# Kernel tuning notes

Measured on AMD Instinct MI355X. Metric: run time of the kernel, lower is better.

Reference implementation:

```python
import jax, jax.numpy as jnp
import numpy as np

EPS_DIST = 1e-8
EPS_BN = 1e-5


def _bn_relu(x, g, b):
    # training-mode BatchNorm1d over (batch, spatial) per channel, then ReLU
    mean = jnp.mean(x, axis=(0, 2), keepdims=True)
    var = jnp.mean((x - mean) ** 2, axis=(0, 2), keepdims=True)
    xhat = (x - mean) * jax.lax.rsqrt(var + EPS_BN)
    return jax.nn.relu(xhat * g[None, :, None] + b[None, :, None])


def setup_inputs() -> dict:
    key = jax.random.key(0)
    ks = jax.random.split(key, 8)
    B, N, M, C1, C2 = 8, 16384, 4096, 64, 256
    return {
        "p1": jax.random.normal(ks[0], (B, N, 3), jnp.float32),
        "p2": jax.random.normal(ks[1], (B, M, 3), jnp.float32),
        "f1": jax.random.normal(ks[2], (B, C1, N), jnp.float32),
        "f2": jax.random.normal(ks[3], (B, C2, M), jnp.float32),
        "idx": jax.random.randint(ks[4], (B, N, 3), 0, M, jnp.int64),
        "W1": jax.random.normal(ks[5], (256, C1 + C2), jnp.float32) * 0.05,
        "g1": jnp.ones((256,), jnp.float32),
        "b1": jnp.zeros((256,), jnp.float32),
        "W2": jax.random.normal(ks[6], (256, 256), jnp.float32) * 0.05,
        "g2": jnp.ones((256,), jnp.float32),
        "b2": jnp.zeros((256,), jnp.float32),
    }


def reference(p1, p2, f1, f2, idx, W1, g1, b1, W2, g2, b2):
    B = p1.shape[0]
    b_ix = jnp.arange(B)[:, None, None]  # batch index for gathers
    # --- three_interpolation: inverse-squared-distance weighted 3-NN interp ---
    nbr_xyz = p2[b_ix, idx]                     # [B, N, 3, 3]
    d2 = jnp.sum((p1[:, :, None, :] - nbr_xyz) ** 2, axis=-1)  # [B, N, 3]
    recip = 1.0 / (d2 + EPS_DIST)
    weight = recip / jnp.sum(recip, axis=-1, keepdims=True)    # [B, N, 3]
    f2_nbr = jnp.swapaxes(f2, 1, 2)[b_ix, idx]  # [B, N, 3, C2]
    interp = jnp.einsum("bnkc,bnk->bcn", f2_nbr, weight)       # [B, C2, N]
    # --- concat + two 1x1 conv + BN + ReLU blocks ---
    x = jnp.concatenate((f1, interp), axis=1)   # [B, C1+C2, N]
    x = _bn_relu(jnp.einsum("oi,bin->bon", W1, x), g1, b1)
    x = _bn_relu(jnp.einsum("oi,bin->bon", W2, x), g2, b2)
    return x
```

## Files before the change

### kernel.cpp

```cpp
#include <hip/hip_runtime.h>
#include <hip/hip_bf16.h>

#define BB 8
#define NN 16384
#define MM 4096
#define C1 64
#define C2 256
#define K1 320
#define CO 256
#define MTOT (BB * NN)

#define STATS_OFF 0
#define FLAG_OFF  8192
#define W1B_OFF   16384
#define W2B_OFF   180224
#define F2T_OFF   327680
#define XT_OFF    (327680 + 16777216)
#define H2_OFF    (327680 + 16777216 + 83886080)


typedef short v8s __attribute__((ext_vector_type(8)));
typedef float v4f __attribute__((ext_vector_type(4)));

__device__ __forceinline__ float bf2f(unsigned short u) {
    unsigned v = ((unsigned)u) << 16;
    float f;
    __builtin_memcpy(&f, &v, 4);
    return f;
}
__device__ __forceinline__ unsigned short f2bf(float f) {
    unsigned u;
    __builtin_memcpy(&u, &f, 4);
    unsigned r = u + 0x7fffu + ((u >> 16) & 1u);
    return (unsigned short)(r >> 16);
}
__device__ __forceinline__ void gload16(const unsigned short* g, unsigned short* l) {
    __builtin_amdgcn_global_load_lds((const __attribute__((address_space(1))) unsigned int*)g,
                                     (__attribute__((address_space(3))) unsigned int*)l, 16, 0, 0);
}

__global__ void k_prep(const void* idx_raw, int* flag64, float* stats,
                       const float* __restrict__ W1, unsigned short* __restrict__ W1b,
                       const float* __restrict__ W2, unsigned short* __restrict__ W2b) {
    int blk = blockIdx.x;
    int t = threadIdx.x;
    if (blk < 320) {
        int e = blk * 256 + t;
        int row = e / K1, col = e - row * K1;
        W1b[row * K1 + (col ^ ((row & 7) << 3))] = f2bf(W1[e]);
    } else if (blk < 576) {
        int e = (blk - 320) * 256 + t;
        int row = e >> 8, col = e & 255;
        W2b[row * CO + (col ^ ((row & 7) << 3))] = f2bf(W2[e]);
    } else {
        for (int i = t; i < 8 * 256; i += 256) stats[i] = 0.f;
        if (t == 0) {
            const int* a = (const int*)idx_raw;
            int all0 = 1;
            for (int j = 1; j < 64; j += 2) all0 &= (a[j] == 0);
            *flag64 = all0;
        }
    }
}

__global__ void k_tr_f2(const float* __restrict__ f2, unsigned short* __restrict__ f2t) {
    __shared__ float tile[64][33];
    int b = blockIdx.z;
    int c0 = blockIdx.y * 64;
    int m0 = blockIdx.x * 32;
    int t = threadIdx.x;
    int lm = t & 31, lc = t >> 5;
    const float* src = f2 + ((size_t)b * C2 + c0) * MM + m0;
#pragma unroll
    for (int j = 0; j < 8; ++j)
        tile[lc + 8 * j][lm] = src[(size_t)(lc + 8 * j) * MM + lm];
    __syncthreads();
    int m = t >> 3, c8 = (t & 7) * 8;
    unsigned short tmp[8];
#pragma unroll
    for (int k = 0; k < 8; ++k) tmp[k] = f2bf(tile[c8 + k][m]);
    uint4 v;
    v.x = (unsigned)tmp[0] | ((unsigned)tmp[1] << 16);
    v.y = (unsigned)tmp[2] | ((unsigned)tmp[3] << 16);
    v.z = (unsigned)tmp[4] | ((unsigned)tmp[5] << 16);
    v.w = (unsigned)tmp[6] | ((unsigned)tmp[7] << 16);
    *(uint4*)&f2t[((size_t)b * MM + m0 + m) * C2 + c0 + c8] = v;
}

__global__ void k_tr_f1(const float* __restrict__ f1, unsigned short* __restrict__ xT) {
    __shared__ float tile[64][33];
    int b = blockIdx.z;
    int n0 = blockIdx.x * 32;
    int t = threadIdx.x;
    int lm = t & 31, lc = t >> 5;
    const float* src = f1 + ((size_t)b * C1) * NN + n0;
#pragma unroll
    for (int j = 0; j < 8; ++j)
        tile[lc + 8 * j][lm] = src[(size_t)(lc + 8 * j) * NN + lm];
    __syncthreads();
    int m = t >> 3, c8 = (t & 7) * 8;
    unsigned short tmp[8];
#pragma unroll
    for (int k = 0; k < 8; ++k) tmp[k] = f2bf(tile[c8 + k][m]);
    uint4 v;
    v.x = (unsigned)tmp[0] | ((unsigned)tmp[1] << 16);
    v.y = (unsigned)tmp[2] | ((unsigned)tmp[3] << 16);
    v.z = (unsigned)tmp[4] | ((unsigned)tmp[5] << 16);
    v.w = (unsigned)tmp[6] | ((unsigned)tmp[7] << 16);
    *(uint4*)&xT[((size_t)b * NN + n0 + m) * K1 + (c8 ^ ((m & 7) * 8))] = v;
}

__global__ void k_interp(const float* __restrict__ p1, const float* __restrict__ p2,
                         const void* __restrict__ idxv, const int* __restrict__ flag64,
                         const unsigned short* __restrict__ f2t,
                         unsigned short* __restrict__ xT) {
    int t = threadIdx.x;
    int p = t >> 5, lane = t & 31;
    size_t pt = (size_t)blockIdx.x * 8 + p;
    int b = (int)(pt >> 14);
    int m0, m1, m2;
    if (*flag64) {
        const long long* id = (const long long*)idxv;
        m0 = (int)id[pt * 3 + 0]; m1 = (int)id[pt * 3 + 1]; m2 = (int)id[pt * 3 + 2];
    } else {
        const int* id = (const int*)idxv;
        m0 = id[pt * 3 + 0]; m1 = id[pt * 3 + 1]; m2 = id[pt * 3 + 2];
    }
    float qx = p1[pt * 3 + 0], qy = p1[pt * 3 + 1], qz = p1[pt * 3 + 2];
    const float* pb = p2 + (size_t)b * MM * 3;
    float dx, dy, dz;
    dx = qx - pb[m0 * 3 + 0]; dy = qy - pb[m0 * 3 + 1]; dz = qz - pb[m0 * 3 + 2];
    float d0 = dx * dx + dy * dy + dz * dz;
    dx = qx - pb[m1 * 3 + 0]; dy = qy - pb[m1 * 3 + 1]; dz = qz - pb[m1 * 3 + 2];
    float d1 = dx * dx + dy * dy + dz * dz;
    dx = qx - pb[m2 * 3 + 0]; dy = qy - pb[m2 * 3 + 1]; dz = qz - pb[m2 * 3 + 2];
    float d2v = dx * dx + dy * dy + dz * dz;
    float r0 = 1.f / (d0 + 1e-8f), r1 = 1.f / (d1 + 1e-8f), r2 = 1.f / (d2v + 1e-8f);
    float inv = 1.f / (r0 + r1 + r2);
    float w0 = r0 * inv, w1 = r1 * inv, w2 = r2 * inv;

    const unsigned short* fb = f2t + (size_t)b * MM * C2;
    int c0 = lane * 8;
    uint4 va = *(const uint4*)(fb + (size_t)m0 * C2 + c0);
    uint4 vb = *(const uint4*)(fb + (size_t)m1 * C2 + c0);
    uint4 vc = *(const uint4*)(fb + (size_t)m2 * C2 + c0);

    float r[8];
    {
        const unsigned av[4] = {va.x, va.y, va.z, va.w};
        const unsigned bv[4] = {vb.x, vb.y, vb.z, vb.w};
        const unsigned cv[4] = {vc.x, vc.y, vc.z, vc.w};
#pragma unroll
        for (int q = 0; q < 4; ++q) {
            r[2 * q + 0] = w0 * bf2f((unsigned short)(av[q] & 0xffff))
                         + w1 * bf2f((unsigned short)(bv[q] & 0xffff))
                         + w2 * bf2f((unsigned short)(cv[q] & 0xffff));
            r[2 * q + 1] = w0 * bf2f((unsigned short)(av[q] >> 16))
                         + w1 * bf2f((unsigned short)(bv[q] >> 16))
                         + w2 * bf2f((unsigned short)(cv[q] >> 16));
        }
    }
    uint4 outv;
    outv.x = (unsigned)f2bf(r[0]) | ((unsigned)f2bf(r[1]) << 16);
    outv.y = (unsigned)f2bf(r[2]) | ((unsigned)f2bf(r[3]) << 16);
    outv.z = (unsigned)f2bf(r[4]) | ((unsigned)f2bf(r[5]) << 16);
    outv.w = (unsigned)f2bf(r[6]) | ((unsigned)f2bf(r[7]) << 16);
    *(uint4*)(xT + pt * K1 + ((C1 + c0) ^ (((int)pt & 7) * 8))) = outv;
}

#define TM 128
#define TN 128
#define TK 64
__launch_bounds__(256)
__global__ void k_gemm1(const unsigned short* __restrict__ xT,
                        const unsigned short* __restrict__ W1b,
                        unsigned short* __restrict__ h1,
                        float* __restrict__ sum1, float* __restrict__ ssq1) {
    __shared__ unsigned short smem[TM * TK + TN * TK];
    __shared__ float s_sum[TN], s_ssq[TN];
    unsigned short* As = smem;
    unsigned short* Bs = smem + TM * TK;
    const int t = threadIdx.x;
    const int lane = t & 63, w = t >> 6;
    const int wm = w >> 1, wc = w & 1;
    const long rbase = (long)blockIdx.x * TM;
    const int cb = blockIdx.y * TN;

    if (t < TN) { s_sum[t] = 0.f; s_ssq[t] = 0.f; }

    v4f acc[4][4];
#pragma unroll
    for (int r = 0; r < 4; ++r)
#pragma unroll
        for (int c = 0; c < 4; ++c) acc[r][c] = (v4f)(0.f);

    const int srow = w * 32 + (lane >> 3);
    const int sch = (lane & 7) * 8;
    const unsigned short* Ag = xT + (rbase + srow) * K1 + sch;
    const unsigned short* Bg = W1b + (size_t)(cb + srow) * K1 + sch;

    const int ln = lane & 15, q = lane >> 4;
    const int xs = (ln & 7) * 8;

    for (int k0 = 0; k0 < K1; k0 += TK) {
#pragma unroll
        for (int j = 0; j < 4; ++j) {
            gload16(Ag + (size_t)(j * 8) * K1 + k0, As + (w * 32 + j * 8) * TK);
            gload16(Bg + (size_t)(j * 8) * K1 + k0, Bs + (w * 32 + j * 8) * TK);
        }
        __syncthreads();
        const unsigned short* ApL = As + (wm * 64 + ln) * TK;
        const unsigned short* BpL = Bs + (wc * 64 + ln) * TK;
#pragma unroll
        for (int ks = 0; ks < 2; ++ks) {
            const int off = (q * 8 + ks * 32) ^ xs;
            v8s af[4], bg[4];
#pragma unroll
            for (int r = 0; r < 4; ++r) af[r] = *(const v8s*)(ApL + r * 16 * TK + off);
#pragma unroll
            for (int c = 0; c < 4; ++c) bg[c] = *(const v8s*)(BpL + c * 16 * TK + off);
#pragma unroll
            for (int r = 0; r < 4; ++r)
#pragma unroll
                for (int c = 0; c < 4; ++c)
                    acc[r][c] = __builtin_amdgcn_mfma_f32_16x16x32_bf16(af[r], bg[c], acc[r][c], 0, 0, 0);
        }
        __syncthreads();
    }

#pragma unroll
    for (int c = 0; c < 4; ++c) {
        int col = wc * 64 + c * 16 + ln;
        int cc = col >> 3, ci = col & 7;
        float s = 0.f, sq = 0.f;
#pragma unroll
        for (int r = 0; r < 4; ++r)
#pragma unroll
            for (int i = 0; i < 4; ++i) {
                int row = wm * 64 + r * 16 + q * 4 + i;
                float v = acc[r][c][i];
                smem[row * 128 + 8 * (cc ^ (row & 15)) + ci] = f2bf(v);
                s += v; sq += v * v;
            }
        atomicAdd(&s_sum[col], s);
        atomicAdd(&s_ssq[col], sq);
    }
    __syncthreads();
    {
        int rr = t >> 4, cc2 = t & 15;
#pragma unroll
        for (int j = 0; j < 8; ++j) {
            int row = rr + 16 * j;
            uint4 v = *(const uint4*)&smem[row * 128 + 8 * (cc2 ^ (row & 15))];
            *(uint4*)&h1[(size_t)(rbase + row) * CO + cb + cc2 * 8] = v;
        }
    }
    if (t < TN) {
        atomicAdd(&sum1[cb + t], s_sum[t]);
        atomicAdd(&ssq1[cb + t], s_ssq[t]);
    }
}

__launch_bounds__(256)
__global__ void k_gemm2(const unsigned short* __restrict__ h1,
                        const unsigned short* __restrict__ W2b,
                        const float* __restrict__ sum1, const float* __restrict__ ssq1,
                        const float* __restrict__ g1, const float* __restrict__ b1,
                        unsigned short* __restrict__ h2,
                        float* __restrict__ sum2, float* __restrict__ ssq2) {
    __shared__ unsigned short smem[TM * TK + TN * TK];
    __shared__ float s_sum[TN], s_ssq[TN];
    __shared__ float sc1[CO], sh1[CO];
    unsigned short* As = smem;
    unsigned short* Bs = smem + TM * TK;
    const int t = threadIdx.x;
    const int lane = t & 63, w = t >> 6;
    const int wm = w >> 1, wc = w & 1;
    const long rbase = (long)blockIdx.x * TM;
    const int cb = blockIdx.y * TN;

    {
        const float invn = 1.f / (float)MTOT;
        float m = sum1[t] * invn;
        float v = ssq1[t] * invn - m * m;
        float s = g1[t] * rsqrtf(v + 1e-5f);
        sc1[t] = s;
        sh1[t] = b1[t] - m * s;
    }
    if (t < TN) { s_sum[t] = 0.f; s_ssq[t] = 0.f; }
    __syncthreads();

    v4f acc[4][4];
#pragma unroll
    for (int r = 0; r < 4; ++r)
#pragma unroll
        for (int c = 0; c < 4; ++c) acc[r][c] = (v4f)(0.f);

    const int srow = w * 32 + (lane >> 3);
    const int sch = (lane & 7) * 8;
    const unsigned short* Ag = h1 + (rbase + srow) * CO + sch;
    const unsigned short* Bg = W2b + (size_t)(cb + srow) * CO + sch;
    unsigned short* AsW = As + srow * TK + (sch ^ ((srow & 7) * 8));

    for (int k0 = 0; k0 < CO; k0 += TK) {
#pragma unroll
        for (int j = 0; j < 4; ++j)
            gload16(Bg + (size_t)(j * 8) * CO + k0, Bs + (w * 32 + j * 8) * TK);
        float4 sca = *(const float4*)(sc1 + k0 + sch);
        float4 scb = *(const float4*)(sc1 + k0 + sch + 4);
        float4 sha = *(const float4*)(sh1 + k0 + sch);
        float4 shb = *(const float4*)(sh1 + k0 + sch + 4);
#pragma unroll
        for (int j = 0; j < 4; ++j) {
            uint4 av = *(const uint4*)(Ag + (size_t)(j * 8) * CO + k0);
            float y0 = fmaxf(bf2f((unsigned short)(av.x & 0xffff)) * sca.x + sha.x, 0.f);
            float y1 = fmaxf(bf2f((unsigned short)(av.x >> 16)) * sca.y + sha.y, 0.f);
            float y2 = fmaxf(bf2f((unsigned short)(av.y & 0xffff)) * sca.z + sha.z, 0.f);
            float y3 = fmaxf(bf2f((unsigned short)(av.y >> 16)) * sca.w + sha.w, 0.f);
            float y4 = fmaxf(bf2f((unsigned short)(av.z & 0xffff)) * scb.x + shb.x, 0.f);
            float y5 = fmaxf(bf2f((unsigned short)(av.z >> 16)) * scb.y + shb.y, 0.f);
            float y6 = fmaxf(bf2f((unsigned short)(av.w & 0xffff)) * scb.z + shb.z, 0.f);
            float y7 = fmaxf(bf2f((unsigned short)(av.w >> 16)) * scb.w + shb.w, 0.f);
            uint4 ov;
            ov.x = (unsigned)f2bf(y0) | ((unsigned)f2bf(y1) << 16);
            ov.y = (unsigned)f2bf(y2) | ((unsigned)f2bf(y3) << 16);
            ov.z = (unsigned)f2bf(y4) | ((unsigned)f2bf(y5) << 16);
            ov.w = (unsigned)f2bf(y6) | ((unsigned)f2bf(y7) << 16);
            *(uint4*)(AsW + (j * 8) * TK) = ov;
        }
        __syncthreads();
        const int ln = lane & 15, q = lane >> 4;
        const int xs = (ln & 7) * 8;
        const unsigned short* ApL = As + (wm * 64 + ln) * TK;
        const unsigned short* BpL = Bs + (wc * 64 + ln) * TK;
#pragma unroll
        for (int ks = 0; ks < 2; ++ks) {
            const int off = (q * 8 + ks * 32) ^ xs;
            v8s af[4], bg4[4];
#pragma unroll
            for (int r = 0; r < 4; ++r) af[r] = *(const v8s*)(ApL + r * 16 * TK + off);
#pragma unroll
            for (int c = 0; c < 4; ++c) bg4[c] = *(const v8s*)(BpL + c * 16 * TK + off);
#pragma unroll
            for (int r = 0; r < 4; ++r)
#pragma unroll
                for (int c = 0; c < 4; ++c)
                    acc[r][c] = __builtin_amdgcn_mfma_f32_16x16x32_bf16(af[r], bg4[c], acc[r][c], 0, 0, 0);
        }
        __syncthreads();
    }

    const int q = lane >> 4, ln = lane & 15;
    const int b = (int)(rbase >> 14);
    const int nb = (int)(rbase & (NN - 1));
#pragma unroll
    for (int c = 0; c < 4; ++c) {
        int ol = wc * 64 + c * 16 + ln;
        float s = 0.f, sq = 0.f;
#pragma unroll
        for (int r = 0; r < 4; ++r)
#pragma unroll
            for (int i = 0; i < 4; ++i) {
                int row = wm * 64 + r * 16 + q * 4 + i;
                int rc = row >> 3, ri = row & 7;
                float v = acc[r][c][i];
                smem[ol * 128 + 8 * (rc ^ (ol & 15)) + ri] = f2bf(v);
                s += v; sq += v * v;
            }
        atomicAdd(&s_sum[ol], s);
        atomicAdd(&s_ssq[ol], sq);
    }
    __syncthreads();
    {
        int oo = t >> 4, nc = t & 15;
#pragma unroll
        for (int j = 0; j < 8; ++j) {
            int ol = oo + 16 * j;
            uint4 v = *(const uint4*)&smem[ol * 128 + 8 * (nc ^ (ol & 15))];
            *(uint4*)&h2[(((size_t)(b * CO + cb + ol)) << 14) + nb + nc * 8] = v;
        }
    }
    if (t < TN) {
        atomicAdd(&sum2[cb + t], s_sum[t]);
        atomicAdd(&ssq2[cb + t], s_ssq[t]);
    }
}

__global__ void k_apply(const unsigned short* __restrict__ h2,
                        const float* __restrict__ sum2, const float* __restrict__ ssq2,
                        const float* __restrict__ g2, const float* __restrict__ b2,
                        float* __restrict__ out) {
    __shared__ float ss[2];
    int o = (blockIdx.x >> 4) & 255;
    if (threadIdx.x == 0) {
        const float invn = 1.f / (float)MTOT;
        float m = sum2[o] * invn;
        float v = ssq2[o] * invn - m * m;
        float s = g2[o] * rsqrtf(v + 1e-5f);
        ss[0] = s;
        ss[1] = b2[o] - m * s;
    }
    __syncthreads();
    float s = ss[0], d = ss[1];
    size_t i = ((size_t)blockIdx.x * 256 + threadIdx.x) * 4;
    ushort4 hv = *(const ushort4*)(h2 + i);
    float4 v;
    v.x = fmaxf(bf2f(hv.x) * s + d, 0.f);
    v.y = fmaxf(bf2f(hv.y) * s + d, 0.f);
    v.z = fmaxf(bf2f(hv.z) * s + d, 0.f);
    v.w = fmaxf(bf2f(hv.w) * s + d, 0.f);
    *(float4*)&out[i] = v;
}

extern "C" void kernel_launch(void* const* d_in, const int* in_sizes, int n_in,
                              void* d_out, int out_size, void* d_ws, size_t ws_size,
                              hipStream_t stream) {
    const float* p1 = (const float*)d_in[0];
    const float* p2 = (const float*)d_in[1];
    const float* f1 = (const float*)d_in[2];
    const float* f2 = (const float*)d_in[3];
    const void*  idx = d_in[4];
    const float* W1 = (const float*)d_in[5];
    const float* g1 = (const float*)d_in[6];
    const float* b1 = (const float*)d_in[7];
    const float* W2 = (const float*)d_in[8];
    const float* g2 = (const float*)d_in[9];
    const float* b2 = (const float*)d_in[10];
    float* out = (float*)d_out;

    char* ws = (char*)d_ws;
    float* stats = (float*)(ws + STATS_OFF);
    float* sum1 = stats + 0;     float* ssq1 = stats + 256;
    float* sum2 = stats + 1024;  float* ssq2 = stats + 1280;
    int* flag64 = (int*)(ws + FLAG_OFF);
    unsigned short* W1b = (unsigned short*)(ws + W1B_OFF);
    unsigned short* W2b = (unsigned short*)(ws + W2B_OFF);
    unsigned short* f2t = (unsigned short*)(ws + F2T_OFF);
    unsigned short* xT  = (unsigned short*)(ws + XT_OFF);
    unsigned short* h2  = (unsigned short*)(ws + H2_OFF);

    unsigned short* h1 = (unsigned short*)d_out;

    k_prep<<<577, 256, 0, stream>>>(idx, flag64, stats, W1, W1b, W2, W2b);
    k_tr_f2<<<dim3(MM / 32, C2 / 64, BB), 256, 0, stream>>>(f2, f2t);
    k_tr_f1<<<dim3(NN / 32, 1, BB), 256, 0, stream>>>(f1, xT);
    k_interp<<<MTOT / 8, 256, 0, stream>>>(p1, p2, idx, flag64, f2t, xT);
    k_gemm1<<<dim3(MTOT / TM, CO / TN), 256, 0, stream>>>(xT, W1b, h1, sum1, ssq1);
    k_gemm2<<<dim3(MTOT / TM, CO / TN), 256, 0, stream>>>(h1, W2b, sum1, ssq1, g1, b1, h2, sum2, ssq2);
    k_apply<<<(int)((size_t)out_size / 4 / 256), 256, 0, stream>>>(h2, sum2, ssq2, g2, b2, out);
}
```

Baseline: 423.1 us.

## Double-buffer gemm1 LDS tiles, swap grid order, reduce BN stats via shuffles

Double-buffers k_gemm1's shared-memory A/B tiles so the next K-slice loads while the current one feeds MFMA, which also removes one barrier per iteration. Both GEMMs swap grid dimensions so the two column blocks of the same row tile run next to each other and can share the A tile in cache. The LDS atomics for BN statistics are replaced by wavefront shuffle reductions with direct global atomics. This doubles gemm1's LDS use, which may lower occupancy, and issues more global atomics per block.

```diff
diff --git a/kernel.cpp b/kernel.cpp
--- a/kernel.cpp
+++ b/kernel.cpp
@@ -176,17 +176,12 @@
                         const unsigned short* __restrict__ W1b,
                         unsigned short* __restrict__ h1,
                         float* __restrict__ sum1, float* __restrict__ ssq1) {
-    __shared__ unsigned short smem[TM * TK + TN * TK];
-    __shared__ float s_sum[TN], s_ssq[TN];
-    unsigned short* As = smem;
-    unsigned short* Bs = smem + TM * TK;
+    __shared__ unsigned short smem[2][TM * TK + TN * TK];
     const int t = threadIdx.x;
     const int lane = t & 63, w = t >> 6;
     const int wm = w >> 1, wc = w & 1;
-    const long rbase = (long)blockIdx.x * TM;
-    const int cb = blockIdx.y * TN;
-
-    if (t < TN) { s_sum[t] = 0.f; s_ssq[t] = 0.f; }
+    const long rbase = (long)blockIdx.y * TM;
+    const int cb = blockIdx.x * TN;
 
     v4f acc[4][4];
 #pragma unroll
@@ -202,15 +197,24 @@
     const int ln = lane & 15, q = lane >> 4;
     const int xs = (ln & 7) * 8;
 
+#pragma unroll
+    for (int j = 0; j < 4; ++j) {
+        gload16(Ag + (size_t)(j * 8) * K1, smem[0] + (w * 32 + j * 8) * TK);
+        gload16(Bg + (size_t)(j * 8) * K1, smem[0] + TM * TK + (w * 32 + j * 8) * TK);
+    }
+    __syncthreads();
+
     for (int k0 = 0; k0 < K1; k0 += TK) {
-#pragma unroll
-        for (int j = 0; j < 4; ++j) {
-            gload16(Ag + (size_t)(j * 8) * K1 + k0, As + (w * 32 + j * 8) * TK);
-            gload16(Bg + (size_t)(j * 8) * K1 + k0, Bs + (w * 32 + j * 8) * TK);
-        }
-        __syncthreads();
-        const unsigned short* ApL = As + (wm * 64 + ln) * TK;
-        const unsigned short* BpL = Bs + (wc * 64 + ln) * TK;
+        const int p = (k0 >> 6) & 1;
+        if (k0 + TK < K1) {
+#pragma unroll
+            for (int j = 0; j < 4; ++j) {
+                gload16(Ag + (size_t)(j * 8) * K1 + k0 + TK, smem[p ^ 1] + (w * 32 + j * 8) * TK);
+                gload16(Bg + (size_t)(j * 8) * K1 + k0 + TK, smem[p ^ 1] + TM * TK + (w * 32 + j * 8) * TK);
+            }
+        }
+        const unsigned short* ApL = smem[p] + (wm * 64 + ln) * TK;
+        const unsigned short* BpL = smem[p] + TM * TK + (wc * 64 + ln) * TK;
 #pragma unroll
         for (int ks = 0; ks < 2; ++ks) {
             const int off = (q * 8 + ks * 32) ^ xs;
@@ -228,6 +232,7 @@
         __syncthreads();
     }
 
+    unsigned short* ep = (unsigned short*)smem;
 #pragma unroll
     for (int c = 0; c < 4; ++c) {
         int col = wc * 64 + c * 16 + ln;
@@ -239,11 +244,15 @@
             for (int i = 0; i < 4; ++i) {
                 int row = wm * 64 + r * 16 + q * 4 + i;
                 float v = acc[r][c][i];
-                smem[row * 128 + 8 * (cc ^ (row & 15)) + ci] = f2bf(v);
+                ep[row * 128 + 8 * (cc ^ (row & 15)) + ci] = f2bf(v);
                 s += v; sq += v * v;
             }
-        atomicAdd(&s_sum[col], s);
-        atomicAdd(&s_ssq[col], sq);
+        s += __shfl_xor(s, 16); sq += __shfl_xor(sq, 16);
+        s += __shfl_xor(s, 32); sq += __shfl_xor(sq, 32);
+        if (lane < 16) {
+            atomicAdd(&sum1[cb + col], s);
+            atomicAdd(&ssq1[cb + col], sq);
+        }
     }
     __syncthreads();
     {
@@ -251,13 +260,9 @@
 #pragma unroll
         for (int j = 0; j < 8; ++j) {
             int row = rr + 16 * j;
-            uint4 v = *(const uint4*)&smem[row * 128 + 8 * (cc2 ^ (row & 15))];
+            uint4 v = *(const uint4*)&ep[row * 128 + 8 * (cc2 ^ (row & 15))];
             *(uint4*)&h1[(size_t)(rbase + row) * CO + cb + cc2 * 8] = v;
         }
-    }
-    if (t < TN) {
-        atomicAdd(&sum1[cb + t], s_sum[t]);
-        atomicAdd(&ssq1[cb + t], s_ssq[t]);
     }
 }
 
@@ -269,15 +274,14 @@
                         unsigned short* __restrict__ h2,
                         float* __restrict__ sum2, float* __restrict__ ssq2) {
     __shared__ unsigned short smem[TM * TK + TN * TK];
-    __shared__ float s_sum[TN], s_ssq[TN];
     __shared__ float sc1[CO], sh1[CO];
     unsigned short* As = smem;
     unsigned short* Bs = smem + TM * TK;
     const int t = threadIdx.x;
     const int lane = t & 63, w = t >> 6;
     const int wm = w >> 1, wc = w & 1;
-    const long rbase = (long)blockIdx.x * TM;
-    const int cb = blockIdx.y * TN;
+    const long rbase = (long)blockIdx.y * TM;
+    const int cb = blockIdx.x * TN;
 
     {
         const float invn = 1.f / (float)MTOT;
@@ -287,7 +291,6 @@
         sc1[t] = s;
         sh1[t] = b1[t] - m * s;
     }
-    if (t < TN) { s_sum[t] = 0.f; s_ssq[t] = 0.f; }
     __syncthreads();
 
     v4f acc[4][4];
@@ -367,8 +370,12 @@
                 smem[ol * 128 + 8 * (rc ^ (ol & 15)) + ri] = f2bf(v);
                 s += v; sq += v * v;
             }
-        atomicAdd(&s_sum[ol], s);
-        atomicAdd(&s_ssq[ol], sq);
+        s += __shfl_xor(s, 16); sq += __shfl_xor(sq, 16);
+        s += __shfl_xor(s, 32); sq += __shfl_xor(sq, 32);
+        if (lane < 16) {
+            atomicAdd(&sum2[cb + ol], s);
+            atomicAdd(&ssq2[cb + ol], sq);
+        }
     }
     __syncthreads();
     {
@@ -379,10 +386,6 @@
             uint4 v = *(const uint4*)&smem[ol * 128 + 8 * (nc ^ (ol & 15))];
             *(uint4*)&h2[(((size_t)(b * CO + cb + ol)) << 14) + nb + nc * 8] = v;
         }
-    }
-    if (t < TN) {
-        atomicAdd(&sum2[cb + t], s_sum[t]);
-        atomicAdd(&ssq2[cb + t], s_ssq[t]);
     }
 }
 
@@ -445,7 +448,7 @@
     k_tr_f2<<<dim3(MM / 32, C2 / 64, BB), 256, 0, stream>>>(f2, f2t);
     k_tr_f1<<<dim3(NN / 32, 1, BB), 256, 0, stream>>>(f1, xT);
     k_interp<<<MTOT / 8, 256, 0, stream>>>(p1, p2, idx, flag64, f2t, xT);
-    k_gemm1<<<dim3(MTOT / TM, CO / TN), 256, 0, stream>>>(xT, W1b, h1, sum1, ssq1);
-    k_gemm2<<<dim3(MTOT / TM, CO / TN), 256, 0, stream>>>(h1, W2b, sum1, ssq1, g1, b1, h2, sum2, ssq2);
+    k_gemm1<<<dim3(CO / TN, MTOT / TM), 256, 0, stream>>>(xT, W1b, h1, sum1, ssq1);
+    k_gemm2<<<dim3(CO / TN, MTOT / TM), 256, 0, stream>>>(h1, W2b, sum1, ssq1, g1, b1, h2, sum2, ssq2);
     k_apply<<<(int)((size_t)out_size / 4 / 256), 256, 0, stream>>>(h2, sum2, ssq2, g2, b2, out);
 }
```

Result: faster. 405.8 us (-4.1%).
